# Kernel optimization log

Hardware: AMD Instinct MI355X
Metric: run time of the kernel (lower is better)

## Reference

```python
import jax, jax.numpy as jnp
import numpy as np

N = 100000   # num entities / tail rows
D_IN = 128
D_OUT = 128
R = 8        # num relations
E = 131072   # edges per relation
B = 32768    # head entities per relation


def setup_inputs() -> dict:
    key = jax.random.key(0)
    ks = jax.random.split(key, 8)
    x = jax.random.normal(ks[0], (N, D_IN), dtype=jnp.float32)
    tail_rep = jax.random.normal(ks[1], (N, D_IN), dtype=jnp.float32)
    # Linear(in, out, bias=False) weight: [out, in], xavier-ish scale
    W = jax.random.normal(ks[2], (D_OUT, D_IN), dtype=jnp.float32) * (1.414 / np.sqrt(D_IN))
    # match_matrix embedding -> per-relation [in, out] matrices
    rel_W = jax.random.normal(ks[3], (R, D_IN, D_OUT), dtype=jnp.float32) * (1.0 / np.sqrt(D_IN))
    edge_weights = jax.random.uniform(ks[4], (R, E), dtype=jnp.float32)
    edge_rows = jax.random.randint(ks[5], (R, E), 0, B, dtype=jnp.int32)
    edge_cols = jax.random.randint(ks[6], (R, E), 0, N, dtype=jnp.int32)
    # head_indice: unique global entity ids per relation (torch code assigns by index)
    rng = np.random.default_rng(0)
    head = np.stack([rng.choice(N, size=B, replace=False) for _ in range(R)]).astype(np.int32)
    head_indice = jnp.asarray(head)
    return {"x": x, "tail_rep": tail_rep, "W": W, "rel_W": rel_W,
            "edge_weights": edge_weights, "edge_rows": edge_rows,
            "edge_cols": edge_cols, "head_indice": head_indice}


def reference(x, tail_rep, W, rel_W, edge_weights, edge_rows, edge_cols, head_indice):
    # emb_all = original_map(input)
    emb_all = x @ W.T                                   # [N, D_OUT]
    # per-relation dense transform of all tails: tail_rep @ rel_W[r]
    transformed = jnp.einsum('ni,rio->rno', tail_rep, rel_W)   # [R, N, D_OUT]
    # sparse.mm(sp_edge_e, all_rep_h): gather tail rows per edge, weight, segment-sum by local head row
    gathered = jnp.take_along_axis(transformed, edge_cols[:, :, None], axis=1)  # [R, E, D_OUT]
    contrib = edge_weights[:, :, None] * gathered                                # [R, E, D_OUT]
    seg = lambda c, rows: jax.ops.segment_sum(c, rows, num_segments=B)
    new_rep = jax.vmap(seg)(contrib, edge_rows)                                  # [R, B, D_OUT]
    # emb_all[ent_indice] = rel_update + emb_all[ent_indice]  (per relation, sequentially) == scatter-add
    emb_all = emb_all.at[head_indice.reshape(-1)].add(new_rep.reshape(-1, D_OUT))
    # activate=True
    return jax.nn.relu(emb_all)
```

## Files before the change

### kernel.cpp

```cpp
#include <hip/hip_runtime.h>
#include <hip/hip_bf16.h>

#define D_DIM 128
#define N_ENT 100000
#define R_REL 8
#define E_EDGE 131072
#define B_HEAD 32768
#define NH_PAD 100352

typedef __attribute__((ext_vector_type(8))) short short8v;
typedef __attribute__((ext_vector_type(16))) float f32x16;
typedef unsigned int uint;
typedef unsigned short ushort;

union BF8 {
  short8v v;
  __hip_bfloat16 h[8];
};

__device__ inline ushort bfbits(float x) {
  union { __hip_bfloat16 h; ushort u; } c;
  c.h = __float2bfloat16(x);
  return c.u;
}
__device__ inline float bflo(uint p) { return __uint_as_float(p << 16); }
__device__ inline float bfhi(uint p) { return __uint_as_float(p & 0xffff0000u); }

__global__ __launch_bounds__(256) void init_ws(int* __restrict__ cnt_e,
                                               int* __restrict__ inv) {
  int i = blockIdx.x * 256 + threadIdx.x;
  if (i < R_REL * B_HEAD) cnt_e[i] = 0;
  inv[i] = -1;
}

__global__ __launch_bounds__(256) void prep_tail(const float* __restrict__ tail,
                                                 short8v* __restrict__ tailb) {
  int i = blockIdx.x * 256 + threadIdx.x;
  const float4* s = (const float4*)tail + (size_t)i * 2;
  float4 a = s[0], b = s[1];
  BF8 h;
  h.h[0] = __float2bfloat16(a.x); h.h[1] = __float2bfloat16(a.y);
  h.h[2] = __float2bfloat16(a.z); h.h[3] = __float2bfloat16(a.w);
  h.h[4] = __float2bfloat16(b.x); h.h[5] = __float2bfloat16(b.y);
  h.h[6] = __float2bfloat16(b.z); h.h[7] = __float2bfloat16(b.w);
  tailb[i] = h.v;
}

__global__ __launch_bounds__(256) void hist_edges(const int* __restrict__ erow,
                                                  int* __restrict__ cnt) {
  int r = blockIdx.y;
  int e = blockIdx.x * 256 + threadIdx.x;
  int row = erow[(size_t)r * E_EDGE + e];
  atomicAdd(cnt + r * B_HEAD + row, 1);
}

__global__ __launch_bounds__(256) void scan_blk(const int* __restrict__ cnt,
                                                int* __restrict__ cur,
                                                int* __restrict__ bsum) {
  int b = blockIdx.x, t = threadIdx.x;
  int4 v = ((const int4*)cnt)[b * 256 + t];
  int s = v.x + v.y + v.z + v.w;
  __shared__ int ps[256];
  ps[t] = s;
  __syncthreads();
  for (int off = 1; off < 256; off <<= 1) {
    int u = (t >= off) ? ps[t - off] : 0;
    __syncthreads();
    ps[t] += u;
    __syncthreads();
  }
  int base = ps[t] - s;
  int4 o;
  o.x = base; o.y = base + v.x; o.z = o.y + v.y; o.w = o.z + v.z;
  ((int4*)cur)[b * 256 + t] = o;
  if (t == 255) bsum[b] = ps[255];
}

__global__ __launch_bounds__(256) void scan_bsum(int* __restrict__ bsum) {
  int t = threadIdx.x;
  int s = bsum[t];
  __shared__ int ps[256];
  ps[t] = s;
  __syncthreads();
  for (int off = 1; off < 256; off <<= 1) {
    int u = (t >= off) ? ps[t - off] : 0;
    __syncthreads();
    ps[t] += u;
    __syncthreads();
  }
  bsum[t] = ps[t] - s;
}

__global__ __launch_bounds__(256) void scan_add(int* __restrict__ cur,
                                                const int* __restrict__ bsum) {
  int i = blockIdx.x * 256 + threadIdx.x;
  int o = bsum[i >> 8];
  int4 v = ((int4*)cur)[i];
  v.x += o; v.y += o; v.z += o; v.w += o;
  ((int4*)cur)[i] = v;
}

__global__ __launch_bounds__(256) void scatter_edges(const int* __restrict__ erow,
                                                     const int* __restrict__ ecol,
                                                     const float* __restrict__ ew,
                                                     int* __restrict__ cur,
                                                     int2* __restrict__ sColW) {
  int r = blockIdx.y;
  int e = blockIdx.x * 256 + threadIdx.x;
  size_t idx = (size_t)r * E_EDGE + e;
  int row = erow[idx];
  int pos = atomicAdd(cur + r * B_HEAD + row, 1);
  sColW[pos] = make_int2(ecol[idx], __float_as_int(ew[idx]));
}

__global__ __launch_bounds__(256) void build_inv(const int* __restrict__ head,
                                                 int* __restrict__ inv) {
  int i = blockIdx.x * 256 + threadIdx.x;
  int r = i >> 15;
  inv[r * NH_PAD + head[i]] = i & (B_HEAD - 1);
}

__global__ __launch_bounds__(256) void csr_agg(const uint* __restrict__ tailb,
                                               const int* __restrict__ end_e,
                                               const int* __restrict__ cnt_e,
                                               const int2* __restrict__ sColW,
                                               uint* __restrict__ aggb, int r0) {
  int wid = (blockIdx.x << 2) + (threadIdx.x >> 6);
  int lane = threadIdx.x & 63;
  int f = r0 * B_HEAD + wid;
  int cn = cnt_e[f];
  int s = end_e[f] - cn;
  float ax = 0.f, ay = 0.f, bx = 0.f, by = 0.f;
  int k = 0;
  for (; k + 2 <= cn; k += 2) {
    int2 e0 = sColW[s + k];
    int2 e1 = sColW[s + k + 1];
    uint t0 = tailb[(size_t)e0.x * 64 + lane];
    uint t1 = tailb[(size_t)e1.x * 64 + lane];
    float w0 = __int_as_float(e0.y), w1 = __int_as_float(e1.y);
    ax += w0 * bflo(t0); ay += w0 * bfhi(t0);
    bx += w1 * bflo(t1); by += w1 * bfhi(t1);
  }
  if (k < cn) {
    int2 e0 = sColW[s + k];
    uint t0 = tailb[(size_t)e0.x * 64 + lane];
    float w0 = __int_as_float(e0.y);
    ax += w0 * bflo(t0); ay += w0 * bfhi(t0);
  }
  ax += bx; ay += by;
  aggb[(size_t)wid * 64 + lane] = (uint)bfbits(ax) | ((uint)bfbits(ay) << 16);
}

__global__ __launch_bounds__(256) void prep_W(const float* __restrict__ W,
                                              const float* __restrict__ relW,
                                              short8v* __restrict__ WhS,
                                              short8v* __restrict__ WlS) {
  int mat = blockIdx.y;
  int idx = blockIdx.x * 256 + threadIdx.x;
  int o = idx & 127, ks = idx >> 7;
  float v[8];
  if (mat == 0) {
    const float* src = W + o * D_DIM + ks * 8;
#pragma unroll
    for (int j = 0; j < 8; ++j) v[j] = src[j];
  } else {
    const float* src = relW + (size_t)(mat - 1) * D_DIM * D_DIM + (ks * 8) * D_DIM + o;
#pragma unroll
    for (int j = 0; j < 8; ++j) v[j] = src[j * D_DIM];
  }
  BF8 h, l;
#pragma unroll
  for (int j = 0; j < 8; ++j) {
    __hip_bfloat16 hb = __float2bfloat16(v[j]);
    h.h[j] = hb;
    l.h[j] = __float2bfloat16(v[j] - __bfloat162float(hb));
  }
  WhS[(size_t)mat * 2048 + idx] = h.v;
  WlS[(size_t)mat * 2048 + idx] = l.v;
}

__global__ __launch_bounds__(256) void gemm_rel(const ushort* __restrict__ aggb,
                                                const short8v* __restrict__ WhS,
                                                const short8v* __restrict__ WlS,
                                                ushort* __restrict__ updb, int r0) {
  __shared__ short8v wlds[2][8][128];
  int tid = threadIdx.x;
  int kk_rel = blockIdx.y;
  int mat = 1 + r0 + kk_rel;
  const short8v* Hsrc = WhS + (size_t)mat * 2048;
  const short8v* Lsrc = WlS + (size_t)mat * 2048;
  int w = tid >> 6, lane = tid & 63, lrow = lane & 31, lsel = lane >> 5;
  int arow = blockIdx.x * 128 + w * 32 + lrow;
  const short8v* Arow =
      (const short8v*)(aggb + ((size_t)kk_rel * B_HEAD + arow) * D_DIM);

  f32x16 acc[4] = {};
  for (int half = 0; half < 2; ++half) {
    if (half) __syncthreads();
#pragma unroll
    for (int it = 0; it < 4; ++it) {
      int e = it * 256 + tid;
      wlds[0][e >> 7][e & 127] = Hsrc[half * 1024 + e];
      wlds[1][e >> 7][e & 127] = Lsrc[half * 1024 + e];
    }
    __syncthreads();
#pragma unroll
    for (int kk = 0; kk < 4; ++kk) {
      short8v a = Arow[half * 8 + kk * 2 + lsel];
      int ks = kk * 2 + lsel;
#pragma unroll
      for (int n = 0; n < 4; ++n) {
        short8v bh = wlds[0][ks][n * 32 + lrow];
        short8v bl = wlds[1][ks][n * 32 + lrow];
        acc[n] = __builtin_amdgcn_mfma_f32_32x32x16_bf16(a, bh, acc[n], 0, 0, 0);
        acc[n] = __builtin_amdgcn_mfma_f32_32x32x16_bf16(a, bl, acc[n], 0, 0, 0);
      }
    }
  }
  int wrow0 = blockIdx.x * 128 + w * 32;
#pragma unroll
  for (int reg = 0; reg < 16; ++reg) {
    int srow = wrow0 + (reg & 3) + 8 * (reg >> 2) + 4 * lsel;
    ushort* urow = updb + ((size_t)kk_rel * B_HEAD + srow) * D_DIM;
#pragma unroll
    for (int n = 0; n < 4; ++n) urow[n * 32 + lrow] = bfbits(acc[n][reg]);
  }
}

template <bool FUSE>
__global__ __launch_bounds__(256) void gemm_x(const float* __restrict__ A,
                                              const short8v* __restrict__ WhS,
                                              const short8v* __restrict__ WlS,
                                              const int* __restrict__ inv,
                                              const ushort* __restrict__ updb,
                                              float* __restrict__ Out, int nrows) {
  __shared__ short8v wlds[2][8][128];
  int tid = threadIdx.x;
  int w = tid >> 6, lane = tid & 63, lrow = lane & 31, lsel = lane >> 5;
  int arow = blockIdx.x * 128 + w * 32 + lrow;
  int arowc = (arow < nrows) ? arow : (nrows - 1);
  const float4* Arow = (const float4*)(A + (size_t)arowc * D_DIM);

  f32x16 acc[4] = {};
  for (int half = 0; half < 2; ++half) {
    if (half) __syncthreads();
#pragma unroll
    for (int it = 0; it < 4; ++it) {
      int e = it * 256 + tid;
      wlds[0][e >> 7][e & 127] = WhS[half * 1024 + e];
      wlds[1][e >> 7][e & 127] = WlS[half * 1024 + e];
    }
    __syncthreads();
#pragma unroll
    for (int kk = 0; kk < 4; ++kk) {
      int k0 = half * 64 + kk * 16;
      float4 a0 = Arow[(k0 >> 2) + lsel * 2];
      float4 a1 = Arow[(k0 >> 2) + lsel * 2 + 1];
      float av[8] = {a0.x, a0.y, a0.z, a0.w, a1.x, a1.y, a1.z, a1.w};
      BF8 ah, al;
#pragma unroll
      for (int j = 0; j < 8; ++j) {
        __hip_bfloat16 hb = __float2bfloat16(av[j]);
        ah.h[j] = hb;
        al.h[j] = __float2bfloat16(av[j] - __bfloat162float(hb));
      }
      int ks = kk * 2 + lsel;
#pragma unroll
      for (int n = 0; n < 4; ++n) {
        short8v bh = wlds[0][ks][n * 32 + lrow];
        short8v bl = wlds[1][ks][n * 32 + lrow];
        acc[n] = __builtin_amdgcn_mfma_f32_32x32x16_bf16(ah.v, bh, acc[n], 0, 0, 0);
        acc[n] = __builtin_amdgcn_mfma_f32_32x32x16_bf16(ah.v, bl, acc[n], 0, 0, 0);
        acc[n] = __builtin_amdgcn_mfma_f32_32x32x16_bf16(al.v, bh, acc[n], 0, 0, 0);
        acc[n] = __builtin_amdgcn_mfma_f32_32x32x16_bf16(al.v, bl, acc[n], 0, 0, 0);
      }
    }
  }
  int wrow0 = blockIdx.x * 128 + w * 32;
#pragma unroll
  for (int reg = 0; reg < 16; ++reg) {
    int srow = wrow0 + (reg & 3) + 8 * (reg >> 2) + 4 * lsel;
    if (srow < nrows) {
      float vals[4];
#pragma unroll
      for (int n = 0; n < 4; ++n) vals[n] = acc[n][reg];
      if (FUSE) {
#pragma unroll
        for (int r = 0; r < R_REL; ++r) {
          int row = inv[r * NH_PAD + srow];
          if (row >= 0) {
            const ushort* u = updb + ((size_t)r * B_HEAD + row) * D_DIM;
#pragma unroll
            for (int n = 0; n < 4; ++n)
              vals[n] += __uint_as_float((uint)u[n * 32 + lrow] << 16);
          }
        }
#pragma unroll
        for (int n = 0; n < 4; ++n) vals[n] = fmaxf(vals[n], 0.f);
      }
      float* orow = Out + (size_t)srow * D_DIM;
#pragma unroll
      for (int n = 0; n < 4; ++n) orow[n * 32 + lrow] = vals[n];
    }
  }
}

__global__ __launch_bounds__(256) void final_add(const int* __restrict__ inv,
                                                 const ushort* __restrict__ updb,
                                                 float* __restrict__ out, int r0,
                                                 int c, int doRelu) {
  int n = blockIdx.x * 8 + (threadIdx.x >> 5);
  int lane = threadIdx.x & 31;
  if (n >= N_ENT) return;
  float4* o4 = (float4*)out + (size_t)n * 32 + lane;
  float4 v = *o4;
  for (int k = 0; k < c; ++k) {
    int row = inv[(r0 + k) * NH_PAD + n];
    if (row >= 0) {
      uint2 u = ((const uint2*)updb)[((size_t)k * B_HEAD + row) * 32 + lane];
      v.x += bflo(u.x); v.y += bfhi(u.x);
      v.z += bflo(u.y); v.w += bfhi(u.y);
    }
  }
  if (doRelu) {
    v.x = fmaxf(v.x, 0.f); v.y = fmaxf(v.y, 0.f);
    v.z = fmaxf(v.z, 0.f); v.w = fmaxf(v.w, 0.f);
  }
  *o4 = v;
}

extern "C" void kernel_launch(void* const* d_in, const int* in_sizes, int n_in,
                              void* d_out, int out_size, void* d_ws, size_t ws_size,
                              hipStream_t stream) {
  const float* x = (const float*)d_in[0];
  const float* tail = (const float*)d_in[1];
  const float* W = (const float*)d_in[2];
  const float* relW = (const float*)d_in[3];
  const float* ew = (const float*)d_in[4];
  const int* erow = (const int*)d_in[5];
  const int* ecol = (const int*)d_in[6];
  const int* head = (const int*)d_in[7];
  float* out = (float*)d_out;

  char* p = (char*)d_ws;
  short8v* WhS = (short8v*)p;  p += (size_t)(R_REL + 1) * 2048 * 16;
  short8v* WlS = (short8v*)p;  p += (size_t)(R_REL + 1) * 2048 * 16;
  short8v* tailb = (short8v*)p; p += (size_t)N_ENT * D_DIM * 2;
  int* cnt_e = (int*)p;        p += (size_t)R_REL * B_HEAD * 4;
  int* cur_e = (int*)p;        p += (size_t)R_REL * B_HEAD * 4;
  int* inv = (int*)p;          p += (size_t)R_REL * NH_PAD * 4;
  int* bsum = (int*)p;         p += 256 * 4;
  int2* sColW = (int2*)p;      p += (size_t)R_REL * E_EDGE * 8;
  char* dyn = p;
  size_t fixed = (size_t)(p - (char*)d_ws);
  size_t per_rel = (size_t)B_HEAD * D_DIM * 2 * 2;
  size_t avail = (ws_size > fixed) ? ws_size - fixed : 0;
  int chunk = (int)(avail / per_rel);
  if (chunk > R_REL) chunk = R_REL;
  if (chunk < 1) chunk = 1;
  ushort* aggb = (ushort*)dyn;
  ushort* updb = (ushort*)(dyn + (size_t)chunk * B_HEAD * D_DIM * 2);

  init_ws<<<dim3(R_REL * NH_PAD / 256), 256, 0, stream>>>(cnt_e, inv);
  prep_W<<<dim3(8, R_REL + 1), 256, 0, stream>>>(W, relW, WhS, WlS);
  prep_tail<<<dim3(N_ENT * D_DIM / 8 / 256), 256, 0, stream>>>(tail, tailb);

  hist_edges<<<dim3(E_EDGE / 256, R_REL), 256, 0, stream>>>(erow, cnt_e);
  scan_blk<<<dim3(256), 256, 0, stream>>>(cnt_e, cur_e, bsum);
  scan_bsum<<<dim3(1), 256, 0, stream>>>(bsum);
  scan_add<<<dim3(256), 256, 0, stream>>>(cur_e, bsum);
  scatter_edges<<<dim3(E_EDGE / 256, R_REL), 256, 0, stream>>>(erow, ecol, ew, cur_e,
                                                               sColW);
  build_inv<<<dim3(R_REL * B_HEAD / 256), 256, 0, stream>>>(head, inv);

  if (chunk == R_REL) {
    csr_agg<<<dim3(R_REL * B_HEAD / 4), 256, 0, stream>>>(
        (const uint*)tailb, cur_e, cnt_e, sColW, (uint*)aggb, 0);
    gemm_rel<<<dim3(B_HEAD / 128, R_REL), 256, 0, stream>>>(aggb, WhS, WlS, updb, 0);
    gemm_x<true><<<dim3((N_ENT + 127) / 128), 256, 0, stream>>>(x, WhS, WlS, inv,
                                                                updb, out, N_ENT);
  } else {
    gemm_x<false><<<dim3((N_ENT + 127) / 128), 256, 0, stream>>>(x, WhS, WlS, inv,
                                                                 updb, out, N_ENT);
    for (int r0 = 0; r0 < R_REL; r0 += chunk) {
      int c = (R_REL - r0 < chunk) ? (R_REL - r0) : chunk;
      csr_agg<<<dim3(c * B_HEAD / 4), 256, 0, stream>>>(
          (const uint*)tailb, cur_e, cnt_e, sColW, (uint*)aggb, r0);
      gemm_rel<<<dim3(B_HEAD / 128, c), 256, 0, stream>>>(aggb, WhS, WlS, updb, r0);
      final_add<<<dim3((N_ENT + 7) / 8), 256, 0, stream>>>(inv, updb, out, r0, c,
                                                           (r0 + c == R_REL) ? 1 : 0);
    }
  }
}
```

Measured before the change: 387.0 us.

## Merge x-GEMM into relation GEMM launch and pre-convert x to bf16

Pre-converts x to bf16 in a separate pass and drops the low-order correction term for x, cutting the x GEMM from four MFMAs to two per step. The x GEMM and the per-relation GEMMs now run as one launch with a partitioned block index. The old fused epilogue that added updates and applied relu inside gemm_x is replaced by an always-run final_add pass. This trades an extra conversion pass and a separate read-modify-write of the output for fewer MFMAs and one fewer launch, and lowers the precision of the x product.

New measurement: 329.2 us. 1.18x faster.

```diff
diff --git a/kernel.cpp b/kernel.cpp
--- a/kernel.cpp
+++ b/kernel.cpp
@@ -33,17 +33,17 @@
   inv[i] = -1;
 }
 
-__global__ __launch_bounds__(256) void prep_tail(const float* __restrict__ tail,
-                                                 short8v* __restrict__ tailb) {
+__global__ __launch_bounds__(256) void prep_bf16(const float* __restrict__ src,
+                                                 short8v* __restrict__ dst) {
   int i = blockIdx.x * 256 + threadIdx.x;
-  const float4* s = (const float4*)tail + (size_t)i * 2;
+  const float4* s = (const float4*)src + (size_t)i * 2;
   float4 a = s[0], b = s[1];
   BF8 h;
   h.h[0] = __float2bfloat16(a.x); h.h[1] = __float2bfloat16(a.y);
   h.h[2] = __float2bfloat16(a.z); h.h[3] = __float2bfloat16(a.w);
   h.h[4] = __float2bfloat16(b.x); h.h[5] = __float2bfloat16(b.y);
   h.h[6] = __float2bfloat16(b.z); h.h[7] = __float2bfloat16(b.w);
-  tailb[i] = h.v;
+  dst[i] = h.v;
 }
 
 __global__ __launch_bounds__(256) void hist_edges(const int* __restrict__ erow,
@@ -179,20 +179,37 @@
   WlS[(size_t)mat * 2048 + idx] = l.v;
 }
 
-__global__ __launch_bounds__(256) void gemm_rel(const ushort* __restrict__ aggb,
+__global__ __launch_bounds__(256) void gemm_all(const ushort* __restrict__ xb,
+                                                const ushort* __restrict__ aggb,
                                                 const short8v* __restrict__ WhS,
                                                 const short8v* __restrict__ WlS,
-                                                ushort* __restrict__ updb, int r0) {
+                                                float* __restrict__ out,
+                                                ushort* __restrict__ updb, int r0,
+                                                int nxb) {
   __shared__ short8v wlds[2][8][128];
   int tid = threadIdx.x;
-  int kk_rel = blockIdx.y;
-  int mat = 1 + r0 + kk_rel;
+  int bid = blockIdx.x;
+  bool xpart = (bid < nxb);
+  const ushort* Abase;
+  int mat, rowbase, relloc = 0;
+  if (xpart) {
+    Abase = xb;
+    mat = 0;
+    rowbase = bid * 128;
+  } else {
+    int b = bid - nxb;
+    relloc = b >> 8;
+    mat = 1 + r0 + relloc;
+    rowbase = (b & 255) * 128;
+    Abase = aggb + (size_t)relloc * B_HEAD * D_DIM;
+  }
   const short8v* Hsrc = WhS + (size_t)mat * 2048;
   const short8v* Lsrc = WlS + (size_t)mat * 2048;
   int w = tid >> 6, lane = tid & 63, lrow = lane & 31, lsel = lane >> 5;
-  int arow = blockIdx.x * 128 + w * 32 + lrow;
-  const short8v* Arow =
-      (const short8v*)(aggb + ((size_t)kk_rel * B_HEAD + arow) * D_DIM);
+  int nrows = xpart ? N_ENT : B_HEAD;
+  int arow = rowbase + w * 32 + lrow;
+  int arowc = (arow < nrows) ? arow : (nrows - 1);
+  const short8v* Arow = (const short8v*)(Abase + (size_t)arowc * D_DIM);
 
   f32x16 acc[4] = {};
   for (int half = 0; half < 2; ++half) {
@@ -217,90 +234,25 @@
       }
     }
   }
-  int wrow0 = blockIdx.x * 128 + w * 32;
-#pragma unroll
-  for (int reg = 0; reg < 16; ++reg) {
-    int srow = wrow0 + (reg & 3) + 8 * (reg >> 2) + 4 * lsel;
-    ushort* urow = updb + ((size_t)kk_rel * B_HEAD + srow) * D_DIM;
-#pragma unroll
-    for (int n = 0; n < 4; ++n) urow[n * 32 + lrow] = bfbits(acc[n][reg]);
-  }
-}
-
-template <bool FUSE>
-__global__ __launch_bounds__(256) void gemm_x(const float* __restrict__ A,
-                                              const short8v* __restrict__ WhS,
-                                              const short8v* __restrict__ WlS,
-                                              const int* __restrict__ inv,
-                                              const ushort* __restrict__ updb,
-                                              float* __restrict__ Out, int nrows) {
-  __shared__ short8v wlds[2][8][128];
-  int tid = threadIdx.x;
-  int w = tid >> 6, lane = tid & 63, lrow = lane & 31, lsel = lane >> 5;
-  int arow = blockIdx.x * 128 + w * 32 + lrow;
-  int arowc = (arow < nrows) ? arow : (nrows - 1);
-  const float4* Arow = (const float4*)(A + (size_t)arowc * D_DIM);
-
-  f32x16 acc[4] = {};
-  for (int half = 0; half < 2; ++half) {
-    if (half) __syncthreads();
-#pragma unroll
-    for (int it = 0; it < 4; ++it) {
-      int e = it * 256 + tid;
-      wlds[0][e >> 7][e & 127] = WhS[half * 1024 + e];
-      wlds[1][e >> 7][e & 127] = WlS[half * 1024 + e];
-    }
-    __syncthreads();
-#pragma unroll
-    for (int kk = 0; kk < 4; ++kk) {
-      int k0 = half * 64 + kk * 16;
-      float4 a0 = Arow[(k0 >> 2) + lsel * 2];
-      float4 a1 = Arow[(k0 >> 2) + lsel * 2 + 1];
-      float av[8] = {a0.x, a0.y, a0.z, a0.w, a1.x, a1.y, a1.z, a1.w};
-      BF8 ah, al;
-#pragma unroll
-      for (int j = 0; j < 8; ++j) {
-        __hip_bfloat16 hb = __float2bfloat16(av[j]);
-        ah.h[j] = hb;
-        al.h[j] = __float2bfloat16(av[j] - __bfloat162float(hb));
+  int wrow0 = rowbase + w * 32;
+  if (xpart) {
+#pragma unroll
+    for (int reg = 0; reg < 16; ++reg) {
+      int srow = wrow0 + (reg & 3) + 8 * (reg >> 2) + 4 * lsel;
+      if (srow < N_ENT) {
+        float* orow = out + (size_t)srow * D_DIM;
+#pragma unroll
+        for (int n = 0; n < 4; ++n) orow[n * 32 + lrow] = acc[n][reg];
       }
-      int ks = kk * 2 + lsel;
-#pragma unroll
-      for (int n = 0; n < 4; ++n) {
-        short8v bh = wlds[0][ks][n * 32 + lrow];
-        short8v bl = wlds[1][ks][n * 32 + lrow];
-        acc[n] = __builtin_amdgcn_mfma_f32_32x32x16_bf16(ah.v, bh, acc[n], 0, 0, 0);
-        acc[n] = __builtin_amdgcn_mfma_f32_32x32x16_bf16(ah.v, bl, acc[n], 0, 0, 0);
-        acc[n] = __builtin_amdgcn_mfma_f32_32x32x16_bf16(al.v, bh, acc[n], 0, 0, 0);
-        acc[n] = __builtin_amdgcn_mfma_f32_32x32x16_bf16(al.v, bl, acc[n], 0, 0, 0);
-      }
-    }
-  }
-  int wrow0 = blockIdx.x * 128 + w * 32;
-#pragma unroll
-  for (int reg = 0; reg < 16; ++reg) {
-    int srow = wrow0 + (reg & 3) + 8 * (reg >> 2) + 4 * lsel;
-    if (srow < nrows) {
-      float vals[4];
-#pragma unroll
-      for (int n = 0; n < 4; ++n) vals[n] = acc[n][reg];
-      if (FUSE) {
-#pragma unroll
-        for (int r = 0; r < R_REL; ++r) {
-          int row = inv[r * NH_PAD + srow];
-          if (row >= 0) {
-            const ushort* u = updb + ((size_t)r * B_HEAD + row) * D_DIM;
-#pragma unroll
-            for (int n = 0; n < 4; ++n)
-              vals[n] += __uint_as_float((uint)u[n * 32 + lrow] << 16);
-          }
-        }
-#pragma unroll
-        for (int n = 0; n < 4; ++n) vals[n] = fmaxf(vals[n], 0.f);
-      }
-      float* orow = Out + (size_t)srow * D_DIM;
-#pragma unroll
-      for (int n = 0; n < 4; ++n) orow[n * 32 + lrow] = vals[n];
+    }
+  } else {
+    ushort* ubase = updb + (size_t)relloc * B_HEAD * D_DIM;
+#pragma unroll
+    for (int reg = 0; reg < 16; ++reg) {
+      int srow = wrow0 + (reg & 3) + 8 * (reg >> 2) + 4 * lsel;
+      ushort* urow = ubase + (size_t)srow * D_DIM;
+#pragma unroll
+      for (int n = 0; n < 4; ++n) urow[n * 32 + lrow] = bfbits(acc[n][reg]);
     }
   }
 }
@@ -343,14 +295,15 @@
   float* out = (float*)d_out;
 
   char* p = (char*)d_ws;
-  short8v* WhS = (short8v*)p;  p += (size_t)(R_REL + 1) * 2048 * 16;
-  short8v* WlS = (short8v*)p;  p += (size_t)(R_REL + 1) * 2048 * 16;
+  short8v* WhS = (short8v*)p;   p += (size_t)(R_REL + 1) * 2048 * 16;
+  short8v* WlS = (short8v*)p;   p += (size_t)(R_REL + 1) * 2048 * 16;
   short8v* tailb = (short8v*)p; p += (size_t)N_ENT * D_DIM * 2;
-  int* cnt_e = (int*)p;        p += (size_t)R_REL * B_HEAD * 4;
-  int* cur_e = (int*)p;        p += (size_t)R_REL * B_HEAD * 4;
-  int* inv = (int*)p;          p += (size_t)R_REL * NH_PAD * 4;
-  int* bsum = (int*)p;         p += 256 * 4;
-  int2* sColW = (int2*)p;      p += (size_t)R_REL * E_EDGE * 8;
+  short8v* xb = (short8v*)p;    p += (size_t)N_ENT * D_DIM * 2;
+  int* cnt_e = (int*)p;         p += (size_t)R_REL * B_HEAD * 4;
+  int* cur_e = (int*)p;         p += (size_t)R_REL * B_HEAD * 4;
+  int* inv = (int*)p;           p += (size_t)R_REL * NH_PAD * 4;
+  int* bsum = (int*)p;          p += 256 * 4;
+  int2* sColW = (int2*)p;       p += (size_t)R_REL * E_EDGE * 8;
   char* dyn = p;
   size_t fixed = (size_t)(p - (char*)d_ws);
   size_t per_rel = (size_t)B_HEAD * D_DIM * 2 * 2;
@@ -361,9 +314,12 @@
   ushort* aggb = (ushort*)dyn;
   ushort* updb = (ushort*)(dyn + (size_t)chunk * B_HEAD * D_DIM * 2);
 
+  const int NXB = (N_ENT + 127) / 128;
+
   init_ws<<<dim3(R_REL * NH_PAD / 256), 256, 0, stream>>>(cnt_e, inv);
   prep_W<<<dim3(8, R_REL + 1), 256, 0, stream>>>(W, relW, WhS, WlS);
-  prep_tail<<<dim3(N_ENT * D_DIM / 8 / 256), 256, 0, stream>>>(tail, tailb);
+  prep_bf16<<<dim3(N_ENT * D_DIM / 8 / 256), 256, 0, stream>>>(tail, tailb);
+  prep_bf16<<<dim3(N_ENT * D_DIM / 8 / 256), 256, 0, stream>>>(x, xb);
 
   hist_edges<<<dim3(E_EDGE / 256, R_REL), 256, 0, stream>>>(erow, cnt_e);
   scan_blk<<<dim3(256), 256, 0, stream>>>(cnt_e, cur_e, bsum);
@@ -373,22 +329,14 @@
                                                                sColW);
   build_inv<<<dim3(R_REL * B_HEAD / 256), 256, 0, stream>>>(head, inv);
 
-  if (chunk == R_REL) {
-    csr_agg<<<dim3(R_REL * B_HEAD / 4), 256, 0, stream>>>(
-        (const uint*)tailb, cur_e, cnt_e, sColW, (uint*)aggb, 0);
-    gemm_rel<<<dim3(B_HEAD / 128, R_REL), 256, 0, stream>>>(aggb, WhS, WlS, updb, 0);
-    gemm_x<true><<<dim3((N_ENT + 127) / 128), 256, 0, stream>>>(x, WhS, WlS, inv,
-                                                                updb, out, N_ENT);
-  } else {
-    gemm_x<false><<<dim3((N_ENT + 127) / 128), 256, 0, stream>>>(x, WhS, WlS, inv,
-                                                                 updb, out, N_ENT);
-    for (int r0 = 0; r0 < R_REL; r0 += chunk) {
-      int c = (R_REL - r0 < chunk) ? (R_REL - r0) : chunk;
-      csr_agg<<<dim3(c * B_HEAD / 4), 256, 0, stream>>>(
-          (const uint*)tailb, cur_e, cnt_e, sColW, (uint*)aggb, r0);
-      gemm_rel<<<dim3(B_HEAD / 128, c), 256, 0, stream>>>(aggb, WhS, WlS, updb, r0);
-      final_add<<<dim3((N_ENT + 7) / 8), 256, 0, stream>>>(inv, updb, out, r0, c,
-                                                           (r0 + c == R_REL) ? 1 : 0);
-    }
-  }
-}
+  for (int r0 = 0; r0 < R_REL; r0 += chunk) {
+    int c = (R_REL - r0 < chunk) ? (R_REL - r0) : chunk;
+    csr_agg<<<dim3(c * B_HEAD / 4), 256, 0, stream>>>(
+        (const uint*)tailb, cur_e, cnt_e, sColW, (uint*)aggb, r0);
+    int nxb = (r0 == 0) ? NXB : 0;
+    gemm_all<<<dim3(nxb + 256 * c), 256, 0, stream>>>(
+        (const ushort*)xb, aggb, WhS, WlS, out, updb, r0, nxb);
+    final_add<<<dim3((N_ENT + 7) / 8), 256, 0, stream>>>(inv, updb, out, r0, c,
+                                                         (r0 + c == R_REL) ? 1 : 0);
+  }
+}
```
